# Optimization experiments

Measured on AMD Instinct MI355X. Metric: run time of the kernel, lower is better.

## Reference

```python
import jax, jax.numpy as jnp
import numpy as np

DIM = 768
NUM_EXPERTS = 64
N_FRQ = 2048
TOPK = 2
B = 32
ALPHA = 300.0


def setup_inputs() -> dict:
    key = jax.random.key(0)
    k1, k2, k3, k4 = jax.random.split(key, 4)
    cls_token = jax.random.normal(k1, (B, DIM), dtype=jnp.float32)
    W_router = jax.random.normal(k2, (NUM_EXPERTS, DIM), dtype=jnp.float32) * 0.02
    b_router = jnp.zeros((NUM_EXPERTS,), dtype=jnp.float32)
    coeff = jax.random.normal(k3, (NUM_EXPERTS, N_FRQ), dtype=jnp.float32)
    # distinct flat indices into the dim*dim grid (mirrors torch.randperm slices)
    perm = jax.random.permutation(k4, DIM * DIM)
    list_indices = perm[: NUM_EXPERTS * N_FRQ].reshape(NUM_EXPERTS, N_FRQ).astype(jnp.int32)
    return {
        "cls_token": cls_token,
        "W_router": W_router,
        "b_router": b_router,
        "coeff": coeff,
        "list_indices": list_indices,
    }


def reference(cls_token, W_router, b_router, coeff, list_indices):
    # router + topk expert selection
    logits = cls_token @ W_router.T + b_router                  # [B, E]
    probs = jax.nn.softmax(logits, axis=-1)
    w, idx = jax.lax.top_k(probs, TOPK)                          # [B, topk]
    w = w / jnp.sum(w, axis=-1, keepdims=True)

    # gather per-expert frequency indices and coefficients
    sel_idx = list_indices[idx]                                  # [B, topk, n_frq]
    vals = coeff[idx] * w[..., None]                             # [B, topk, n_frq]

    # scatter-add into flat frequency grid
    b_ix = jnp.arange(B)[:, None, None]                          # [B,1,1]
    mask = jnp.zeros((B, DIM * DIM), dtype=cls_token.dtype)
    mask = mask.at[b_ix, sel_idx].add(vals)
    mask = mask.reshape(B, DIM, DIM)

    # dense inverse FFT2 over the (mostly-zero) grid
    out = jnp.fft.ifft2(mask, axes=(-2, -1)).real * ALPHA        # [B, dim, dim]
    return out
```

## Files before the change

### kernel.cpp

```cpp
#include <hip/hip_runtime.h>
#include <hip/hip_bf16.h>

#define DIM 768
#define NE 64
#define NFRQ 2048
#define NB 32
#define HALF 384
#define KROW 1536
#define KG 768
#define TWO_PI 6.283185307179586f
#define INV768 (1.0f / 768.0f)
#define SCALE (300.0f / (float)(DIM * DIM))

typedef __attribute__((ext_vector_type(8))) short bf16x8;
typedef __attribute__((ext_vector_type(4))) float f32x4;

__global__ __launch_bounds__(256) void prep_kernel(const float* __restrict__ cls,
                                                   const float* __restrict__ W,
                                                   const float* __restrict__ bias,
                                                   const float* __restrict__ coeff,
                                                   const int* __restrict__ lidx,
                                                   int* __restrict__ row_start,
                                                   float2* __restrict__ s_cv,
                                                   __hip_bfloat16* __restrict__ A,
                                                   float2* __restrict__ T2) {
  int bid = blockIdx.x;
  int tid = threadIdx.x;

  if (bid >= 32 + 2 * 192) {
    int c = bid - (32 + 2 * 192);
    for (int x = tid; x < HALF; x += 256) {
      float prod = (float)(c * x);
      float f, sn, cs;
      float rev = prod * INV768;
      asm("v_fract_f32 %0, %1" : "=v"(f) : "v"(rev));
      asm("v_sin_f32 %0, %1" : "=v"(sn) : "v"(f));
      asm("v_cos_f32 %0, %1" : "=v"(cs) : "v"(f));
      T2[(size_t)c * HALF + x] = make_float2(cs, -sn);
    }
    return;
  }
  if (bid >= 32) {
    int idx = bid - 32;
    int y = 2 * (idx % 192) + (idx / 192);
    if (tid < 96) {
      int r0 = tid * 4;
      union { __hip_bfloat16 h[4]; ushort4 v; } uc, us;
#pragma unroll
      for (int j = 0; j < 4; ++j) {
        int m = (y * (r0 + j)) % DIM;
        float s, c;
        sincosf((TWO_PI / (float)DIM) * (float)m, &s, &c);
        uc.h[j] = __float2bfloat16(c);
        us.h[j] = __float2bfloat16(s);
      }
      *(ushort4*)(A + (size_t)idx * KG + r0)        = uc.v;
      *(ushort4*)(A + (size_t)idx * KG + HALF + r0) = us.v;
    }
    return;
  }

  int b = bid;
  __shared__ int cnt[DIM];
  __shared__ int base[DIM];
  __shared__ int wsum[4];
  __shared__ int sel_i[2];
  __shared__ float sel_f[2];
  float* part   = (float*)cnt;
  float* logits = (float*)base;

  {
    int e = tid & 63, q = tid >> 6;
    const float* c = cls + b * DIM + q * 192;
    const float* w = W + e * DIM + q * 192;
    float acc = 0.f;
#pragma unroll 4
    for (int i = 0; i < 192; i += 4) {
      float4 cv4 = *(const float4*)(c + i);
      float4 wv4 = *(const float4*)(w + i);
      acc += cv4.x * wv4.x + cv4.y * wv4.y + cv4.z * wv4.z + cv4.w * wv4.w;
    }
    part[q * 64 + e] = acc;
    __syncthreads();
    if (tid < NE)
      logits[tid] = part[tid] + part[64 + tid] + part[128 + tid] + part[192 + tid] + bias[tid];
    __syncthreads();
    if (tid == 0) {
      int i0 = 0; float l0 = logits[0];
      for (int i = 1; i < NE; ++i) { float v = logits[i]; if (v > l0) { l0 = v; i0 = i; } }
      int i1 = -1; float l1 = -3.4e38f;
      for (int i = 0; i < NE; ++i) {
        if (i == i0) continue;
        float v = logits[i]; if (v > l1) { l1 = v; i1 = i; }
      }
      float w0 = 1.f / (1.f + expf(l1 - l0));
      sel_i[0] = i0; sel_i[1] = i1;
      sel_f[0] = w0; sel_f[1] = 1.f - w0;
    }
    __syncthreads();
  }
  int e0 = sel_i[0], e1 = sel_i[1];
  float w0 = sel_f[0], w1 = sel_f[1];

  for (int i = tid; i < DIM; i += 256) cnt[i] = 0;
  __syncthreads();
  for (int k = tid; k < 2 * NFRQ; k += 256) {
    int t = k >> 11, j = k & (NFRQ - 1);
    int e = t ? e1 : e0;
    int f = lidx[e * NFRQ + j];
    atomicAdd(&cnt[f / DIM], 1);
  }
  __syncthreads();
  {
    int s0 = cnt[3 * tid], s1 = cnt[3 * tid + 1], s2 = cnt[3 * tid + 2];
    int sum = s0 + s1 + s2;
    int lane = tid & 63, wid = tid >> 6;
    int v = sum;
#pragma unroll
    for (int d = 1; d < 64; d <<= 1) {
      int u = __shfl_up(v, d);
      if (lane >= d) v += u;
    }
    if (lane == 63) wsum[wid] = v;
    __syncthreads();
    int woff = 0;
#pragma unroll
    for (int w = 0; w < 4; ++w) if (w < wid) woff += wsum[w];
    int excl = woff + v - sum;
    int* rsg = row_start + b * (DIM + 1);
    base[3 * tid]     = excl;
    base[3 * tid + 1] = excl + s0;
    base[3 * tid + 2] = excl + s0 + s1;
    rsg[3 * tid]     = excl;
    rsg[3 * tid + 1] = excl + s0;
    rsg[3 * tid + 2] = excl + s0 + s1;
    if (tid == 255) rsg[DIM] = excl + sum;
  }
  __syncthreads();
  for (int i = tid; i < DIM; i += 256) cnt[i] = 0;
  __syncthreads();
  for (int k = tid; k < 2 * NFRQ; k += 256) {
    int t = k >> 11, j = k & (NFRQ - 1);
    int e = t ? e1 : e0;
    float w = t ? w1 : w0;
    int f = lidx[e * NFRQ + j];
    int r = f / DIM, c = f - r * DIM;
    int pos = base[r] + atomicAdd(&cnt[r], 1);
    s_cv[b * 4096 + pos] = make_float2(__uint_as_float((unsigned)c * 3072u),
                                       coeff[e * NFRQ + j] * w * SCALE);
  }
}

__global__ __launch_bounds__(256) void stage1_kernel(const int* __restrict__ row_start,
                                                     const float2* __restrict__ s_cv,
                                                     const float2* __restrict__ T2,
                                                     __hip_bfloat16* __restrict__ BT) {
  int b = blockIdx.y;
  int rg = blockIdx.x;
  int tid = threadIdx.x;
  int lane = tid & 63, w = tid >> 6;
  __shared__ __hip_bfloat16 lreP[8][HALF];
  __shared__ __hip_bfloat16 limP[8][HALF];
  __shared__ __hip_bfloat16 lreM[8][HALF];
  __shared__ __hip_bfloat16 limM[8][HALF];
  const int* rs = row_start + b * (DIM + 1);
  const float2* cv = s_cv + b * 4096;
  __hip_bfloat16* BTb = BT + (size_t)b * HALF * KROW;
  int rowBase = rg * 8;

#pragma unroll
  for (int rr = 0; rr < 2; ++rr) {
    int rslot = 2 * w + rr;
    int rp = rowBase + rslot;
    int sA = rs[rp],       eA = rs[rp + 1];
    int sB = rs[rp + 384], eB = rs[rp + 385];
    float accA[12], accB[12];
#pragma unroll
    for (int k = 0; k < 12; ++k) { accA[k] = 0.f; accB[k] = 0.f; }

    int pa = sA, pb = sB;
    for (; pa < eA && pb < eB; ++pa, ++pb) {
      float2 a  = cv[pa];
      float2 bq = cv[pb];
      const char* ta = (const char*)T2 + (size_t)__float_as_uint(a.x);
      const char* tb = (const char*)T2 + (size_t)__float_as_uint(bq.x);
      float va = a.y, vb = bq.y;
#pragma unroll
      for (int j = 0; j < 3; ++j) {
        float4 t0 = *(const float4*)(ta + lane * 16 + j * 1024);
        float4 t1 = *(const float4*)(tb + lane * 16 + j * 1024);
        accA[4 * j + 0] += va * t0.x; accB[4 * j + 0] += vb * t1.x;
        accA[4 * j + 1] += va * t0.y; accB[4 * j + 1] += vb * t1.y;
        accA[4 * j + 2] += va * t0.z; accB[4 * j + 2] += vb * t1.z;
        accA[4 * j + 3] += va * t0.w; accB[4 * j + 3] += vb * t1.w;
      }
    }
    for (; pa < eA; ++pa) {
      float2 a = cv[pa];
      const char* ta = (const char*)T2 + (size_t)__float_as_uint(a.x);
      float va = a.y;
#pragma unroll
      for (int j = 0; j < 3; ++j) {
        float4 t0 = *(const float4*)(ta + lane * 16 + j * 1024);
        accA[4 * j + 0] += va * t0.x;
        accA[4 * j + 1] += va * t0.y;
        accA[4 * j + 2] += va * t0.z;
        accA[4 * j + 3] += va * t0.w;
      }
    }
    for (; pb < eB; ++pb) {
      float2 bq = cv[pb];
      const char* tb = (const char*)T2 + (size_t)__float_as_uint(bq.x);
      float vb = bq.y;
#pragma unroll
      for (int j = 0; j < 3; ++j) {
        float4 t1 = *(const float4*)(tb + lane * 16 + j * 1024);
        accB[4 * j + 0] += vb * t1.x;
        accB[4 * j + 1] += vb * t1.y;
        accB[4 * j + 2] += vb * t1.z;
        accB[4 * j + 3] += vb * t1.w;
      }
    }
#pragma unroll
    for (int j = 0; j < 3; ++j) {
      union { __hip_bfloat16 h[2]; unsigned u; } rP, iP, rM, iM;
      rP.h[0] = __float2bfloat16(accA[4 * j + 0] + accB[4 * j + 0]);
      rP.h[1] = __float2bfloat16(accA[4 * j + 2] + accB[4 * j + 2]);
      iP.h[0] = __float2bfloat16(accA[4 * j + 1] + accB[4 * j + 1]);
      iP.h[1] = __float2bfloat16(accA[4 * j + 3] + accB[4 * j + 3]);
      rM.h[0] = __float2bfloat16(accA[4 * j + 0] - accB[4 * j + 0]);
      rM.h[1] = __float2bfloat16(accA[4 * j + 2] - accB[4 * j + 2]);
      iM.h[0] = __float2bfloat16(accA[4 * j + 1] - accB[4 * j + 1]);
      iM.h[1] = __float2bfloat16(accA[4 * j + 3] - accB[4 * j + 3]);
      int x = 2 * lane + 128 * j;
      *(unsigned*)&lreP[rslot][x] = rP.u;
      *(unsigned*)&limP[rslot][x] = iP.u;
      *(unsigned*)&lreM[rslot][x] = rM.u;
      *(unsigned*)&limM[rslot][x] = iM.u;
    }
  }
  __syncthreads();
  for (int x = tid; x < HALF; x += 256) {
    union { ushort h[8]; uint4 v; } uP, vP, uM, vM;
#pragma unroll
    for (int k = 0; k < 8; ++k) {
      uP.h[k] = *(const ushort*)&lreP[k][x];
      vP.h[k] = *(const ushort*)&limP[k][x];
      uM.h[k] = *(const ushort*)&lreM[k][x];
      vM.h[k] = *(const ushort*)&limM[k][x];
    }
    __hip_bfloat16* dst = BTb + (size_t)x * KROW + rowBase;
    *(uint4*)(dst)        = uP.v;
    *(uint4*)(dst + 384)  = vP.v;
    *(uint4*)(dst + 768)  = uM.v;
    *(uint4*)(dst + 1152) = vM.v;
  }
}

__device__ inline void gload_lds16(const void* g, void* l) {
  __builtin_amdgcn_global_load_lds((const __attribute__((address_space(1))) void*)g,
                                   (__attribute__((address_space(3))) void*)l, 16, 0, 0);
}

__global__ __launch_bounds__(256) void gemm_kernel(const __hip_bfloat16* __restrict__ A,
                                                   const __hip_bfloat16* __restrict__ BT,
                                                   const int* __restrict__ row_start,
                                                   const float2* __restrict__ s_cv,
                                                   float* __restrict__ C) {
  int bid = blockIdx.x;
  int tid = threadIdx.x;
  __shared__ __align__(16) __hip_bfloat16 As[4][64 * 32];
  __shared__ __align__(16) __hip_bfloat16 Bs[4][64 * 32];

  if (bid < 4 * NB) {
    int slice = bid & 3, b = bid >> 2;
    float* ob = C + (size_t)b * DIM * DIM;
    if (slice == 3) {
      for (int x = tid; x < HALF; x += 256) {
        const __hip_bfloat16* btx = BT + ((size_t)(b * HALF + x)) * KROW;
        float acc = 0.f;
        for (int r = 0; r < HALF; r += 8) {
          union { uint4 v4; __hip_bfloat16 h[8]; } u;
          u.v4 = *(const uint4*)(btx + r);
#pragma unroll
          for (int q = 0; q < 8; ++q) {
            float v = __bfloat162float(u.h[q]);
            acc += (q & 1) ? -v : v;
          }
        }
        int xm = x ? DIM - x : 0;
        ob[(size_t)HALF * DIM + x]  = acc;
        ob[(size_t)HALF * DIM + xm] = acc;
      }
      return;
    }
    float* Re384 = (float*)As;
    const int* rs = row_start + b * (DIM + 1);
    const float2* cv = s_cv + b * 4096;
    for (int r = tid; r < DIM; r += 256) {
      int s = rs[r], e = rs[r + 1];
      float acc = 0.f;
      for (int p = s; p < e; ++p) {
        float2 c = cv[p];
        int ci = (int)(__float_as_uint(c.x) / 3072u);
        acc += (ci & 1) ? -c.y : c.y;
      }
      Re384[r] = acc;
    }
    __syncthreads();
    int y = slice * 129 + tid;
    if (tid < 129 && y <= HALF) {
      float yf = (float)y;
      float a0 = 0.f, a1 = 0.f, a2 = 0.f, a3 = 0.f;
      for (int r = 0; r < DIM; r += 4) {
        float f0, f1, f2, f3, c0, c1, c2, c3;
        float v0 = (yf * (float)(r + 0)) * INV768;
        float v1 = (yf * (float)(r + 1)) * INV768;
        float v2 = (yf * (float)(r + 2)) * INV768;
        float v3 = (yf * (float)(r + 3)) * INV768;
        asm("v_fract_f32 %0, %1" : "=v"(f0) : "v"(v0));
        asm("v_fract_f32 %0, %1" : "=v"(f1) : "v"(v1));
        asm("v_fract_f32 %0, %1" : "=v"(f2) : "v"(v2));
        asm("v_fract_f32 %0, %1" : "=v"(f3) : "v"(v3));
        asm("v_cos_f32 %0, %1" : "=v"(c0) : "v"(f0));
        asm("v_cos_f32 %0, %1" : "=v"(c1) : "v"(f1));
        asm("v_cos_f32 %0, %1" : "=v"(c2) : "v"(f2));
        asm("v_cos_f32 %0, %1" : "=v"(c3) : "v"(f3));
        a0 += Re384[r + 0] * c0;
        a1 += Re384[r + 1] * c1;
        a2 += Re384[r + 2] * c2;
        a3 += Re384[r + 3] * c3;
      }
      float acc = (a0 + a1) + (a2 + a3);
      int ym = y ? DIM - y : 0;
      ob[(size_t)y  * DIM + HALF] = acc;
      ob[(size_t)ym * DIM + HALF] = acc;
    }
    return;
  }

  int gbid = bid - 4 * NB;
  int swz = (gbid & 7) * 144 + (gbid >> 3);
  int b = swz / 36; int rem = swz - b * 36;
  int par = rem / 18; int r2 = rem - par * 18;
  int bx = r2 / 3, by = r2 % 3;

  float* Cp = C + (size_t)b * DIM * DIM;
  int y0 = by * 64, x0 = bx * 64;

  int wv = tid >> 6, lane = tid & 63;
  int wr = wv >> 1, wc = wv & 1;
  int lhi = lane >> 4, llo = lane & 15;
  int arow = tid >> 2;
  int soff = (((tid & 3) ^ ((tid >> 3) & 3))) * 8;
  int xslot8 = (lhi ^ ((llo >> 1) & 3)) * 8;

  f32x4 acc1[2][2] = {};
  f32x4 acc2[2][2] = {};

  const __hip_bfloat16* Aip = A  + ((size_t)(par * 192 + y0 + arow)) * KG + soff;
  const __hip_bfloat16* Bip = BT + ((size_t)(b * HALF + x0 + arow)) * KROW + par * KG + soff;

  auto stage = [&](int t) {
    int buf = t & 3;
    int kt = t * 32;
    gload_lds16(Aip + kt, As[buf] + tid * 8);
    gload_lds16(Bip + kt, Bs[buf] + tid * 8);
  };
  auto compute = [&](int t, f32x4 (&acc)[2][2]) {
    int buf = t & 3;
    bf16x8 af[2], bfr[2];
#pragma unroll
    for (int i = 0; i < 2; ++i)
      af[i] = *(const bf16x8*)(As[buf] + (wr * 32 + i * 16 + llo) * 32 + xslot8);
#pragma unroll
    for (int j = 0; j < 2; ++j)
      bfr[j] = *(const bf16x8*)(Bs[buf] + (wc * 32 + j * 16 + llo) * 32 + xslot8);
#pragma unroll
    for (int i = 0; i < 2; ++i)
#pragma unroll
      for (int j = 0; j < 2; ++j)
        acc[i][j] = __builtin_amdgcn_mfma_f32_16x16x32_bf16(af[i], bfr[j], acc[i][j], 0, 0, 0);
  };

  stage(0); stage(1); stage(2);

  for (int t = 0; t < 12; ++t) {
    asm volatile("s_waitcnt vmcnt(4)" ::: "memory");
    __builtin_amdgcn_s_barrier();
    __builtin_amdgcn_sched_barrier(0);
    stage(t + 3);
    compute(t, acc1);
  }
  for (int t = 12; t < 21; ++t) {
    asm volatile("s_waitcnt vmcnt(4)" ::: "memory");
    __builtin_amdgcn_s_barrier();
    __builtin_amdgcn_sched_barrier(0);
    stage(t + 3);
    compute(t, acc2);
  }
  asm volatile("s_waitcnt vmcnt(4)" ::: "memory");
  __builtin_amdgcn_s_barrier();
  __builtin_amdgcn_sched_barrier(0);
  compute(21, acc2);
  asm volatile("s_waitcnt vmcnt(2)" ::: "memory");
  __builtin_amdgcn_s_barrier();
  __builtin_amdgcn_sched_barrier(0);
  compute(22, acc2);
  asm volatile("s_waitcnt vmcnt(0)" ::: "memory");
  __builtin_amdgcn_s_barrier();
  __builtin_amdgcn_sched_barrier(0);
  compute(23, acc2);

#pragma unroll
  for (int i = 0; i < 2; ++i) {
#pragma unroll
    for (int j = 0; j < 2; ++j) {
      int x = x0 + wc * 32 + j * 16 + llo;
      int xm = x ? DIM - x : 0;
#pragma unroll
      for (int q = 0; q < 4; ++q) {
        int tt = y0 + wr * 32 + i * 16 + lhi * 4 + q;
        int y = 2 * tt + par;
        int ym = y ? DIM - y : 0;
        float c1 = acc1[i][j][q], c2 = acc2[i][j][q];
        float vd = c1 + c2;
        float vs = c1 - c2;
        Cp[(size_t)y  * DIM + x]  = vd;
        Cp[(size_t)ym * DIM + xm] = vd;
        Cp[(size_t)y  * DIM + xm] = vs;
        Cp[(size_t)ym * DIM + x]  = vs;
      }
    }
  }
}

extern "C" void kernel_launch(void* const* d_in, const int* in_sizes, int n_in,
                              void* d_out, int out_size, void* d_ws, size_t ws_size,
                              hipStream_t stream) {
  const float* cls   = (const float*)d_in[0];
  const float* Wr    = (const float*)d_in[1];
  const float* br    = (const float*)d_in[2];
  const float* coeff = (const float*)d_in[3];
  const int*   lidx  = (const int*)d_in[4];
  float* out = (float*)d_out;

  char* ws = (char*)d_ws;
  int*    row_start = (int*)(ws + 0);
  float2* s_cv      = (float2*)(ws + 98944);
  __hip_bfloat16* A  = (__hip_bfloat16*)(ws + 1147520);
  float2* T2        = (float2*)(ws + 1737344);
  __hip_bfloat16* BT = (__hip_bfloat16*)(ws + 4096640);

  prep_kernel<<<32 + 384 + DIM, 256, 0, stream>>>(cls, Wr, br, coeff, lidx,
                                                  row_start, s_cv, A, T2);
  stage1_kernel<<<dim3(48, NB), 256, 0, stream>>>(row_start, s_cv, T2, BT);
  gemm_kernel<<<4 * NB + 1152, 256, 0, stream>>>(A, BT, row_start, s_cv, out);
}
```

Measured before the change: 115.9 us.

## Switch GEMM to K=64 double-buffered tiles with syncthreads pipeline

Replaces the 4-stage, K=32 LDS pipeline (explicit vmcnt waits and raw barriers) with a 2-stage double buffer using K=64 tiles, each thread issuing two direct-to-LDS loads per operand, and an 8-way XOR swizzle. The loop runs 12 iterations instead of 24, halving barrier count and doubling MFMA work per barrier. Prefetch depth drops from three stages to one, and __syncthreads waits on all outstanding loads, so global latency may be less hidden. The acc1/acc2 split stays at the same K boundary (6 of 12 iterations).

```diff
diff --git a/kernel.cpp b/kernel.cpp
--- a/kernel.cpp
+++ b/kernel.cpp
@@ -269,8 +269,8 @@
                                                    float* __restrict__ C) {
   int bid = blockIdx.x;
   int tid = threadIdx.x;
-  __shared__ __align__(16) __hip_bfloat16 As[4][64 * 32];
-  __shared__ __align__(16) __hip_bfloat16 Bs[4][64 * 32];
+  __shared__ __align__(16) __hip_bfloat16 As[2][64 * 64];
+  __shared__ __align__(16) __hip_bfloat16 Bs[2][64 * 64];
 
   if (bid < 4 * NB) {
     int slice = bid & 3, b = bid >> 2;
@@ -351,66 +351,65 @@
   int wv = tid >> 6, lane = tid & 63;
   int wr = wv >> 1, wc = wv & 1;
   int lhi = lane >> 4, llo = lane & 15;
-  int arow = tid >> 2;
-  int soff = (((tid & 3) ^ ((tid >> 3) & 3))) * 8;
-  int xslot8 = (lhi ^ ((llo >> 1) & 3)) * 8;
+
+  int c0 = tid, c1 = tid + 256;
+  int row0 = c0 >> 3, row1 = c1 >> 3;
+  int so0 = (((c0 & 7) ^ (row0 & 7))) * 8;
+  int so1 = (((c1 & 7) ^ (row1 & 7))) * 8;
 
   f32x4 acc1[2][2] = {};
   f32x4 acc2[2][2] = {};
 
-  const __hip_bfloat16* Aip = A  + ((size_t)(par * 192 + y0 + arow)) * KG + soff;
-  const __hip_bfloat16* Bip = BT + ((size_t)(b * HALF + x0 + arow)) * KROW + par * KG + soff;
-
-  auto stage = [&](int t) {
-    int buf = t & 3;
-    int kt = t * 32;
-    gload_lds16(Aip + kt, As[buf] + tid * 8);
-    gload_lds16(Bip + kt, Bs[buf] + tid * 8);
+  const __hip_bfloat16* A0 = A  + ((size_t)(par * 192 + y0 + row0)) * KG + so0;
+  const __hip_bfloat16* A1 = A  + ((size_t)(par * 192 + y0 + row1)) * KG + so1;
+  const __hip_bfloat16* B0 = BT + ((size_t)(b * HALF + x0 + row0)) * KROW + par * KG + so0;
+  const __hip_bfloat16* B1 = BT + ((size_t)(b * HALF + x0 + row1)) * KROW + par * KG + so1;
+
+  gload_lds16(A0, As[0] + c0 * 8);
+  gload_lds16(A1, As[0] + c1 * 8);
+  gload_lds16(B0, Bs[0] + c0 * 8);
+  gload_lds16(B1, Bs[0] + c1 * 8);
+  __syncthreads();
+
+  auto step = [&](int t, f32x4 (&acc)[2][2], bool last) {
+    int cur = t & 1;
+    if (!last) {
+      int ktn = (t + 1) * 64;
+      gload_lds16(A0 + ktn, As[cur ^ 1] + c0 * 8);
+      gload_lds16(A1 + ktn, As[cur ^ 1] + c1 * 8);
+      gload_lds16(B0 + ktn, Bs[cur ^ 1] + c0 * 8);
+      gload_lds16(B1 + ktn, Bs[cur ^ 1] + c1 * 8);
+    }
+    bf16x8 af[2][2], bfr[2][2];
+#pragma unroll
+    for (int i = 0; i < 2; ++i)
+#pragma unroll
+      for (int kh = 0; kh < 2; ++kh) {
+        int row = wr * 32 + i * 16 + llo;
+        int phys = ((lhi + 4 * kh) ^ (llo & 7)) * 8;
+        af[i][kh] = *(const bf16x8*)(As[cur] + row * 64 + phys);
+      }
+#pragma unroll
+    for (int j = 0; j < 2; ++j)
+#pragma unroll
+      for (int kh = 0; kh < 2; ++kh) {
+        int row = wc * 32 + j * 16 + llo;
+        int phys = ((lhi + 4 * kh) ^ (llo & 7)) * 8;
+        bfr[j][kh] = *(const bf16x8*)(Bs[cur] + row * 64 + phys);
+      }
+#pragma unroll
+    for (int kh = 0; kh < 2; ++kh)
+#pragma unroll
+      for (int i = 0; i < 2; ++i)
+#pragma unroll
+        for (int j = 0; j < 2; ++j)
+          acc[i][j] = __builtin_amdgcn_mfma_f32_16x16x32_bf16(af[i][kh], bfr[j][kh],
+                                                              acc[i][j], 0, 0, 0);
+    if (!last) __syncthreads();
   };
-  auto compute = [&](int t, f32x4 (&acc)[2][2]) {
-    int buf = t & 3;
-    bf16x8 af[2], bfr[2];
-#pragma unroll
-    for (int i = 0; i < 2; ++i)
-      af[i] = *(const bf16x8*)(As[buf] + (wr * 32 + i * 16 + llo) * 32 + xslot8);
-#pragma unroll
-    for (int j = 0; j < 2; ++j)
-      bfr[j] = *(const bf16x8*)(Bs[buf] + (wc * 32 + j * 16 + llo) * 32 + xslot8);
-#pragma unroll
-    for (int i = 0; i < 2; ++i)
-#pragma unroll
-      for (int j = 0; j < 2; ++j)
-        acc[i][j] = __builtin_amdgcn_mfma_f32_16x16x32_bf16(af[i], bfr[j], acc[i][j], 0, 0, 0);
-  };
-
-  stage(0); stage(1); stage(2);
-
-  for (int t = 0; t < 12; ++t) {
-    asm volatile("s_waitcnt vmcnt(4)" ::: "memory");
-    __builtin_amdgcn_s_barrier();
-    __builtin_amdgcn_sched_barrier(0);
-    stage(t + 3);
-    compute(t, acc1);
-  }
-  for (int t = 12; t < 21; ++t) {
-    asm volatile("s_waitcnt vmcnt(4)" ::: "memory");
-    __builtin_amdgcn_s_barrier();
-    __builtin_amdgcn_sched_barrier(0);
-    stage(t + 3);
-    compute(t, acc2);
-  }
-  asm volatile("s_waitcnt vmcnt(4)" ::: "memory");
-  __builtin_amdgcn_s_barrier();
-  __builtin_amdgcn_sched_barrier(0);
-  compute(21, acc2);
-  asm volatile("s_waitcnt vmcnt(2)" ::: "memory");
-  __builtin_amdgcn_s_barrier();
-  __builtin_amdgcn_sched_barrier(0);
-  compute(22, acc2);
-  asm volatile("s_waitcnt vmcnt(0)" ::: "memory");
-  __builtin_amdgcn_s_barrier();
-  __builtin_amdgcn_sched_barrier(0);
-  compute(23, acc2);
+
+  for (int t = 0; t < 6; ++t)  step(t, acc1, false);
+  for (int t = 6; t < 12; ++t) step(t, acc2, t == 11);
 
 #pragma unroll
   for (int i = 0; i < 2; ++i) {
```

New measurement: 113.2 us. -2.3%, faster.
